# Kernel tuning notes

Measured on AMD Instinct MI355X. Metric: run time of the kernel, lower is better.

## Reference

```python
import jax, jax.numpy as jnp
import numpy as np

N_QUBITS = 8
C64 = jnp.complex64

# ---- gate matrices ----

def u3(t, p, l):
    c = jnp.cos(t / 2).astype(C64)
    s = jnp.sin(t / 2).astype(C64)
    ep = jnp.exp(1j * p).astype(C64)
    el = jnp.exp(1j * l).astype(C64)
    return jnp.stack([jnp.stack([c, -el * s]),
                      jnp.stack([ep * s, ep * el * c])])

def ry(t):
    c = jnp.cos(t / 2).astype(C64)
    s = jnp.sin(t / 2).astype(C64)
    return jnp.stack([jnp.stack([c, -s]), jnp.stack([s, c])])

def rz(t):
    e = jnp.exp(-0.5j * t).astype(C64)
    z = jnp.zeros((), C64)
    return jnp.stack([jnp.stack([e, z]), jnp.stack([z, jnp.conj(e)])])

CNOT = jnp.array([[1, 0, 0, 0], [0, 1, 0, 0], [0, 0, 0, 1], [0, 0, 1, 0]], C64)
PX = jnp.array([[0, 1], [1, 0]], C64)
PY = jnp.array([[0, -1j], [1j, 0]], C64)
PZ = jnp.array([[1, 0], [0, -1]], C64)

# ---- batched state-vector gate application; psi: [B] + [2]*8, wire 0 = axis 1 (MSB) ----

def apply_1q(psi, U, w):
    psi = jnp.moveaxis(psi, w + 1, -1)
    psi = psi @ U.T
    return jnp.moveaxis(psi, -1, w + 1)

def apply_2q(psi, U4, w0, w1):
    psi = jnp.moveaxis(psi, (w0 + 1, w1 + 1), (-2, -1))
    sh = psi.shape
    psi = (psi.reshape(sh[:-2] + (4,)) @ U4.T).reshape(sh)
    return jnp.moveaxis(psi, (-2, -1), (w0 + 1, w1 + 1))

def u_su4(psi, p, w0, w1):
    psi = apply_1q(psi, u3(p[0], p[1], p[2]), w0)
    psi = apply_1q(psi, u3(p[3], p[4], p[5]), w1)
    psi = apply_2q(psi, CNOT, w0, w1)
    psi = apply_1q(psi, ry(p[6]), w0)
    psi = apply_1q(psi, rz(p[7]), w1)
    psi = apply_2q(psi, CNOT, w1, w0)
    psi = apply_1q(psi, ry(p[8]), w0)
    psi = apply_2q(psi, CNOT, w0, w1)
    psi = apply_1q(psi, u3(p[9], p[10], p[11]), w0)
    psi = apply_1q(psi, u3(p[12], p[13], p[14]), w1)
    return psi

LAYER1 = [(0, 1), (2, 3), (4, 5), (6, 7), (1, 2), (3, 4), (5, 6), (7, 0)]
LAYER2 = [(2, 4), (6, 0), (0, 2), (4, 6)]
LAYER3 = [(2, 6)]

def expval(psi, ops):
    phi = psi
    for M, w in ops:
        phi = apply_1q(phi, M, w)
    return jnp.real(jnp.sum(jnp.conj(psi) * phi, axis=tuple(range(1, N_QUBITS + 1))))

def circuit(x, weights):
    # amplitude embedding with normalization
    psi = (x / jnp.linalg.norm(x, axis=1, keepdims=True)).astype(C64)
    psi = psi.reshape((x.shape[0],) + (2,) * N_QUBITS)
    npc = 15
    layers = [LAYER1, LAYER1, LAYER2, LAYER2, LAYER3]
    for i, wires in enumerate(layers):
        p = weights[i * npc:(i + 1) * npc]
        for (w0, w1) in wires:
            psi = u_su4(psi, p, w0, w1)
    meas = [
        expval(psi, [(PX, 2)]), expval(psi, [(PY, 2)]), expval(psi, [(PZ, 2)]),
        expval(psi, [(PX, 6)]), expval(psi, [(PY, 6)]), expval(psi, [(PZ, 6)]),
        expval(psi, [(PX, 2), (PX, 6)]),
        expval(psi, [(PY, 2), (PY, 6)]),
        expval(psi, [(PZ, 2), (PZ, 6)]),
    ]
    return jnp.stack(meas, axis=1)  # [B, 9]


def setup_inputs() -> dict:
    key = jax.random.key(0)
    k1, k2 = jax.random.split(key)
    x = jax.random.normal(k1, (8192, 256), dtype=jnp.float32)
    weights = jax.random.normal(k2, (75,), dtype=jnp.float32)
    return {"x": x, "weights": weights}


def reference(x, weights):
    return circuit(x, weights)
```

## Files before the change

kernel.cpp:

```cpp
#include <hip/hip_runtime.h>

typedef float2 c32;

__device__ __forceinline__ c32 cmul(c32 a, c32 b) {
    return make_float2(a.x * b.x - a.y * b.y, a.x * b.y + a.y * b.x);
}
__device__ __forceinline__ c32 cmad(c32 a, c32 b, c32 acc) {
    acc.x = fmaf(a.x, b.x, fmaf(-a.y, b.y, acc.x));
    acc.y = fmaf(a.x, b.y, fmaf(a.y, b.x, acc.y));
    return acc;
}


__device__ __forceinline__ void mk_u3(float th, float ph, float la, c32 U[2][2]) {
    float ct = cosf(0.5f * th), st = sinf(0.5f * th);
    U[0][0] = make_float2(ct, 0.f);
    U[0][1] = make_float2(-cosf(la) * st, -sinf(la) * st);
    U[1][0] = make_float2(cosf(ph) * st, sinf(ph) * st);
    U[1][1] = make_float2(cosf(ph + la) * ct, sinf(ph + la) * ct);
}

__device__ __forceinline__ void lmul_kron(const c32 A[2][2], const c32 B[2][2], c32 m[4]) {
    c32 t[4];
#pragma unroll
    for (int r = 0; r < 4; ++r) {
        c32 acc = make_float2(0.f, 0.f);
#pragma unroll
        for (int k = 0; k < 4; ++k)
            acc = cmad(cmul(A[r >> 1][k >> 1], B[r & 1][k & 1]), m[k], acc);
        t[r] = acc;
    }
#pragma unroll
    for (int r = 0; r < 4; ++r) m[r] = t[r];
}

__global__ void build_gates_kernel(const float* __restrict__ w, c32* __restrict__ mats) {
    const int t = threadIdx.x;
    if (t >= 20) return;
    const int g = t >> 2, c = t & 3;
    const float* p = w + g * 15;
    const int c0 = c >> 1, c1 = c & 1;
    c32 A[2][2], B[2][2], m[4], tmp;

    mk_u3(p[0], p[1], p[2], A);
    mk_u3(p[3], p[4], p[5], B);
#pragma unroll
    for (int r = 0; r < 4; ++r) m[r] = cmul(A[r >> 1][c0], B[r & 1][c1]);
    tmp = m[2]; m[2] = m[3]; m[3] = tmp;
    {
        float cc = cosf(0.5f * p[6]), s = sinf(0.5f * p[6]);
        A[0][0] = make_float2(cc, 0.f); A[0][1] = make_float2(-s, 0.f);
        A[1][0] = make_float2(s, 0.f);  A[1][1] = make_float2(cc, 0.f);
        float cz = cosf(0.5f * p[7]), sz = sinf(0.5f * p[7]);
        B[0][0] = make_float2(cz, -sz); B[0][1] = make_float2(0.f, 0.f);
        B[1][0] = make_float2(0.f, 0.f); B[1][1] = make_float2(cz, sz);
        lmul_kron(A, B, m);
    }
    tmp = m[1]; m[1] = m[3]; m[3] = tmp;
    {
        float cc = cosf(0.5f * p[8]), s = sinf(0.5f * p[8]);
        A[0][0] = make_float2(cc, 0.f); A[0][1] = make_float2(-s, 0.f);
        A[1][0] = make_float2(s, 0.f);  A[1][1] = make_float2(cc, 0.f);
        B[0][0] = make_float2(1.f, 0.f); B[0][1] = make_float2(0.f, 0.f);
        B[1][0] = make_float2(0.f, 0.f); B[1][1] = make_float2(1.f, 0.f);
        lmul_kron(A, B, m);
    }
    tmp = m[2]; m[2] = m[3]; m[3] = tmp;
    mk_u3(p[9], p[10], p[11], A);
    mk_u3(p[12], p[13], p[14], B);
    lmul_kron(A, B, m);
#pragma unroll
    for (int r = 0; r < 4; ++r) mats[g * 16 + r * 4 + c] = m[r];
}


#define STRIDE 516

__device__ __forceinline__ int swz8(int i) { return i ^ (i >> 4); }
__host__ __device__ constexpr int cswz8(int i) { return i ^ (i >> 4); }

template<int P3, int P2, int P1, int P0>
struct BitMap {
    __device__ static int scatterDyn(int v) {
        return (((v >> 3) & 1) << P3) | (((v >> 2) & 1) << P2) |
               (((v >> 1) & 1) << P1) | ((v & 1) << P0);
    }
    static constexpr int scatter(int v) {
        return (((v >> 3) & 1) << P3) | (((v >> 2) & 1) << P2) |
               (((v >> 1) & 1) << P1) | ((v & 1) << P0);
    }
};

using WA = BitMap<7, 6, 5, 4>;  using LA = BitMap<3, 2, 1, 0>;
using WB = BitMap<3, 2, 1, 0>;  using LB = BitMap<7, 6, 5, 4>;
using WC = BitMap<7, 4, 3, 0>;  using LC = BitMap<6, 5, 2, 1>;
using WD = BitMap<7, 5, 3, 1>;  using LD = BitMap<6, 4, 2, 0>;

template<class WO, class LO, class WN, class LN>
__device__ __forceinline__ void transition(c32* sl, int c, c32 s[16]) {
    const int uo = swz8(LO::scatterDyn(c));
#pragma unroll
    for (int r = 0; r < 16; ++r) sl[uo ^ cswz8(WO::scatter(r))] = s[r];
    const int un = swz8(LN::scatterDyn(c));
#pragma unroll
    for (int r = 0; r < 16; ++r) s[r] = sl[un ^ cswz8(WN::scatter(r))];
}

constexpr int freePos(int A, int B, int k) {
    int cnt = 0;
    for (int p = 0; p < 4; ++p)
        if (p != A && p != B) { if (cnt == k) return p; ++cnt; }
    return -1;
}

template<int A, int B>
__device__ __forceinline__ void gate(const c32 m[16], c32 s[16]) {
    constexpr int C0 = freePos(A, B, 0);
    constexpr int C1 = freePos(A, B, 1);
#pragma unroll
    for (int q = 0; q < 4; ++q) {
        const int base = ((q & 1) << C0) | (((q >> 1) & 1) << C1);
        const int i00 = base, i01 = base | (1 << B), i10 = base | (1 << A),
                  i11 = base | (1 << A) | (1 << B);
        c32 a0 = s[i00], a1 = s[i01], a2 = s[i10], a3 = s[i11];
        c32 r0 = cmul(m[0],  a0); r0 = cmad(m[1],  a1, r0); r0 = cmad(m[2],  a2, r0); r0 = cmad(m[3],  a3, r0);
        c32 r1 = cmul(m[4],  a0); r1 = cmad(m[5],  a1, r1); r1 = cmad(m[6],  a2, r1); r1 = cmad(m[7],  a3, r1);
        c32 r2 = cmul(m[8],  a0); r2 = cmad(m[9],  a1, r2); r2 = cmad(m[10], a2, r2); r2 = cmad(m[11], a3, r2);
        c32 r3 = cmul(m[12], a0); r3 = cmad(m[13], a1, r3); r3 = cmad(m[14], a2, r3); r3 = cmad(m[15], a3, r3);
        s[i00] = r0; s[i01] = r1; s[i10] = r2; s[i11] = r3;
    }
}

__device__ __forceinline__ void loadm(const c32* __restrict__ g, int idx, c32 m[16]) {
#pragma unroll
    for (int k = 0; k < 16; ++k) m[k] = g[idx * 16 + k];
}

__global__ __launch_bounds__(64) void sim_kernel(const float* __restrict__ x,
                                                 const c32* __restrict__ gmats,
                                                 float* __restrict__ out) {
    __shared__ c32 TR[4 * STRIDE];
    const int lane = threadIdx.x;
    const int st   = lane >> 4;
    const int c    = lane & 15;
    const int b    = blockIdx.x * 4 + st;

    const float* xb = x + (size_t)b * 256 + c;
    c32 s[16];
    float ss = 0.f;
#pragma unroll
    for (int r = 0; r < 16; ++r) {
        float v = xb[r << 4];
        s[r] = make_float2(v, 0.f);
        ss = fmaf(v, v, ss);
    }
#pragma unroll
    for (int o = 8; o; o >>= 1) ss += __shfl_xor(ss, o, 64);
    const float inv = 1.0f / sqrtf(ss);
#pragma unroll
    for (int r = 0; r < 16; ++r) s[r].x *= inv;

    c32* sl = TR + st * STRIDE;
    c32 m[16];

    loadm(gmats, 0, m);
    gate<3, 2>(m, s); gate<1, 0>(m, s); gate<2, 1>(m, s);
    transition<WA, LA, WB, LB>(sl, c, s);
    gate<3, 2>(m, s); gate<1, 0>(m, s); gate<2, 1>(m, s);
    transition<WB, LB, WC, LC>(sl, c, s);
    gate<2, 1>(m, s); gate<0, 3>(m, s);
    transition<WC, LC, WA, LA>(sl, c, s);
    loadm(gmats, 1, m);
    gate<3, 2>(m, s); gate<1, 0>(m, s); gate<2, 1>(m, s);
    transition<WA, LA, WB, LB>(sl, c, s);
    gate<3, 2>(m, s); gate<1, 0>(m, s); gate<2, 1>(m, s);
    transition<WB, LB, WC, LC>(sl, c, s);
    gate<2, 1>(m, s); gate<0, 3>(m, s);
    transition<WC, LC, WD, LD>(sl, c, s);
    loadm(gmats, 2, m);
    gate<2, 1>(m, s); gate<0, 3>(m, s); gate<3, 2>(m, s); gate<1, 0>(m, s);
    loadm(gmats, 3, m);
    gate<2, 1>(m, s); gate<0, 3>(m, s); gate<3, 2>(m, s); gate<1, 0>(m, s);
    loadm(gmats, 4, m);
    gate<2, 0>(m, s);

    float e0 = 0, e1 = 0, e2 = 0, e3 = 0, e4 = 0, e5 = 0, e6 = 0, e7 = 0, e8 = 0;
#pragma unroll
    for (int q = 0; q < 4; ++q) {
        const int f = ((q & 1) << 1) | ((q & 2) << 2);
        c32 a00 = s[f], a01 = s[f | 1], a10 = s[f | 4], a11 = s[f | 5];
        float n00 = a00.x * a00.x + a00.y * a00.y;
        float n01 = a01.x * a01.x + a01.y * a01.y;
        float n10 = a10.x * a10.x + a10.y * a10.y;
        float n11 = a11.x * a11.x + a11.y * a11.y;
        float z2r = a00.x * a10.x + a00.y * a10.y + a01.x * a11.x + a01.y * a11.y;
        float z2i = a00.x * a10.y - a00.y * a10.x + a01.x * a11.y - a01.y * a11.x;
        float z6r = a00.x * a01.x + a00.y * a01.y + a10.x * a11.x + a10.y * a11.y;
        float z6i = a00.x * a01.y - a00.y * a01.x + a10.x * a11.y - a10.y * a11.x;
        float w1r = a00.x * a11.x + a00.y * a11.y;
        float w2r = a01.x * a10.x + a01.y * a10.y;
        e0 += 2.f * z2r;  e1 += 2.f * z2i;  e2 += n00 + n01 - n10 - n11;
        e3 += 2.f * z6r;  e4 += 2.f * z6i;  e5 += n00 - n01 + n10 - n11;
        e6 += 2.f * (w1r + w2r);  e7 += 2.f * (w2r - w1r);
        e8 += n00 - n01 - n10 + n11;
    }
    float e[9] = {e0, e1, e2, e3, e4, e5, e6, e7, e8};
#pragma unroll
    for (int mm = 0; mm < 9; ++mm) {
        float v = e[mm];
#pragma unroll
        for (int o = 8; o; o >>= 1) v += __shfl_xor(v, o, 64);
        e[mm] = v;
    }
    if (c == 0) {
#pragma unroll
        for (int mm = 0; mm < 9; ++mm) out[b * 9 + mm] = e[mm];
    }
}

extern "C" void kernel_launch(void* const* d_in, const int* in_sizes, int n_in,
                              void* d_out, int out_size, void* d_ws, size_t ws_size,
                              hipStream_t stream) {
    const float* x = (const float*)d_in[0];
    const float* w = (const float*)d_in[1];
    float* out = (float*)d_out;
    c32* mats = (c32*)d_ws;

    hipLaunchKernelGGL(build_gates_kernel, dim3(1), dim3(64), 0, stream, w, mats);

    const int batch = in_sizes[0] / 256;
    const int nblocks = batch / 4;
    hipLaunchKernelGGL(sim_kernel, dim3(nblocks), dim3(64), 0, stream, x, mats, out);
}
```

Baseline: 32.74 us.

## Split each state vector over 32 lanes with 8 register amplitudes and XOR-swizzled transposes

Each batch element's 256 amplitudes are now spread over 32 lanes holding 8 amplitudes each, instead of 16 lanes holding 16. The gate schedule is rebuilt around 3-qubit register windows, with more LDS transpose steps that use per-transition XOR swizzles to avoid bank conflicts. Blocks grow to 256 threads covering 8 samples, with launch bounds set for 4 blocks per CU. The aim is lower register pressure and more threads in flight, at the cost of more shared-memory round trips per sample.

```diff
diff --git a/kernel.cpp b/kernel.cpp
--- a/kernel.cpp
+++ b/kernel.cpp
@@ -74,52 +74,72 @@
 }
 
 
-#define STRIDE 516
-
-__device__ __forceinline__ int swz8(int i) { return i ^ (i >> 4); }
-__host__ __device__ constexpr int cswz8(int i) { return i ^ (i >> 4); }
-
-template<int P3, int P2, int P1, int P0>
-struct BitMap {
-    __device__ static int scatterDyn(int v) {
-        return (((v >> 3) & 1) << P3) | (((v >> 2) & 1) << P2) |
-               (((v >> 1) & 1) << P1) | ((v & 1) << P0);
-    }
-    static constexpr int scatter(int v) {
-        return (((v >> 3) & 1) << P3) | (((v >> 2) & 1) << P2) |
-               (((v >> 1) & 1) << P1) | ((v & 1) << P0);
+template<int P2, int P1, int P0>
+struct Win {
+    static constexpr bool isReg(int p) { return p == P2 || p == P1 || p == P0; }
+    static constexpr int lanePos(int j) {
+        int cnt = 4;
+        for (int p = 7; p >= 0; --p)
+            if (!isReg(p)) { if (cnt == j) return p; --cnt; }
+        return -1;
+    }
+    __device__ __forceinline__ static int lane(int u) {
+        return (((u >> 4) & 1) << lanePos(4)) | (((u >> 3) & 1) << lanePos(3)) |
+               (((u >> 2) & 1) << lanePos(2)) | (((u >> 1) & 1) << lanePos(1)) |
+               ((u & 1) << lanePos(0));
+    }
+    static constexpr int reg(int r) {
+        return (((r >> 2) & 1) << P2) | (((r >> 1) & 1) << P1) | ((r & 1) << P0);
     }
 };
 
-using WA = BitMap<7, 6, 5, 4>;  using LA = BitMap<3, 2, 1, 0>;
-using WB = BitMap<3, 2, 1, 0>;  using LB = BitMap<7, 6, 5, 4>;
-using WC = BitMap<7, 4, 3, 0>;  using LC = BitMap<6, 5, 2, 1>;
-using WD = BitMap<7, 5, 3, 1>;  using LD = BitMap<6, 4, 2, 0>;
-
-template<class WO, class LO, class WN, class LN>
-__device__ __forceinline__ void transition(c32* sl, int c, c32 s[16]) {
-    const int uo = swz8(LO::scatterDyn(c));
-#pragma unroll
-    for (int r = 0; r < 16; ++r) sl[uo ^ cswz8(WO::scatter(r))] = s[r];
-    const int un = swz8(LN::scatterDyn(c));
-#pragma unroll
-    for (int r = 0; r < 16; ++r) s[r] = sl[un ^ cswz8(WN::scatter(r))];
-}
-
-constexpr int freePos(int A, int B, int k) {
-    int cnt = 0;
-    for (int p = 0; p < 4; ++p)
-        if (p != A && p != B) { if (cnt == k) return p; ++cnt; }
-    return -1;
+using WA_ = Win<7, 6, 5>;
+using WB_ = Win<6, 3, 2>;
+using WC_ = Win<7, 1, 0>;
+using WD_ = Win<5, 4, 3>;
+using WE_ = Win<7, 2, 1>;
+using WF_ = Win<6, 5, 3>;
+using WG_ = Win<7, 3, 1>;
+using WH_ = Win<7, 5, 3>;
+using WI_ = Win<7, 5, 1>;
+
+template<int S0, int T0, int S1, int T1, int S2, int T2, int S3, int T3>
+struct XF {
+    __device__ static constexpr int enc(int a) {
+        int x = a ^ (((a >> S0) & 1) << T0);
+        if constexpr (S1 >= 0) x ^= ((a >> S1) & 1) << T1;
+        if constexpr (S2 >= 0) x ^= ((a >> S2) & 1) << T2;
+        if constexpr (S3 >= 0) x ^= ((a >> S3) & 1) << T3;
+        return x;
+    }
+};
+using X1  = XF<7,3, 4,2, -1,-1, -1,-1>;
+using X2  = XF<7,3, 5,2, 6,1, 4,0>;
+using X3  = XF<7,3, 6,1, 5,0, -1,-1>;
+using X4  = XF<7,3, 5,2, 6,1, -1,-1>;
+using X5  = XF<4,2, 5,1, -1,-1, -1,-1>;
+using X10 = XF<7,3, 4,2, 5,1, -1,-1>;
+using X11 = XF<4,3, 6,1, -1,-1, -1,-1>;
+using X12 = XF<6,3, 4,1, -1,-1, -1,-1>;
+using X13 = XF<6,3, 5,1, -1,-1, -1,-1>;
+using X14 = XF<6,3, 4,1, -1,-1, -1,-1>;
+
+template<class WO, class WN, class X>
+__device__ __forceinline__ void trans(c32* sl, int u, c32 s[8]) {
+    const int lo = X::enc(WO::lane(u));
+#pragma unroll
+    for (int r = 0; r < 8; ++r) sl[lo ^ X::enc(WO::reg(r))] = s[r];
+    const int ln = X::enc(WN::lane(u));
+#pragma unroll
+    for (int r = 0; r < 8; ++r) s[r] = sl[ln ^ X::enc(WN::reg(r))];
 }
 
 template<int A, int B>
-__device__ __forceinline__ void gate(const c32 m[16], c32 s[16]) {
-    constexpr int C0 = freePos(A, B, 0);
-    constexpr int C1 = freePos(A, B, 1);
-#pragma unroll
-    for (int q = 0; q < 4; ++q) {
-        const int base = ((q & 1) << C0) | (((q >> 1) & 1) << C1);
+__device__ __forceinline__ void gate8(const c32 m[16], c32 s[8]) {
+    constexpr int Cb = 3 - A - B;
+#pragma unroll
+    for (int q = 0; q < 2; ++q) {
+        const int base = q << Cb;
         const int i00 = base, i01 = base | (1 << B), i10 = base | (1 << A),
                   i11 = base | (1 << A) | (1 << B);
         c32 a0 = s[i00], a1 = s[i01], a2 = s[i10], a3 = s[i11];
@@ -136,59 +156,83 @@
     for (int k = 0; k < 16; ++k) m[k] = g[idx * 16 + k];
 }
 
-__global__ __launch_bounds__(64) void sim_kernel(const float* __restrict__ x,
-                                                 const c32* __restrict__ gmats,
-                                                 float* __restrict__ out) {
-    __shared__ c32 TR[4 * STRIDE];
-    const int lane = threadIdx.x;
-    const int st   = lane >> 4;
-    const int c    = lane & 15;
-    const int b    = blockIdx.x * 4 + st;
-
-    const float* xb = x + (size_t)b * 256 + c;
-    c32 s[16];
+__global__ __launch_bounds__(256, 4) void sim_kernel(const float* __restrict__ x,
+                                                     const c32* __restrict__ gmats,
+                                                     float* __restrict__ out) {
+    __shared__ c32 TR[8 * 256];
+    const int tid = threadIdx.x;
+    const int wv = tid >> 6, lane = tid & 63;
+    const int st = lane >> 5, u = lane & 31;
+    const int slot = (wv << 1) | st;
+    const int b = blockIdx.x * 8 + slot;
+    c32* sl = TR + slot * 256;
+
+    const float* xr = x + (size_t)b * 256;
+    c32 s[8];
     float ss = 0.f;
 #pragma unroll
-    for (int r = 0; r < 16; ++r) {
-        float v = xb[r << 4];
+    for (int r = 0; r < 8; ++r) {
+        float v = xr[(r << 5) | u];
         s[r] = make_float2(v, 0.f);
         ss = fmaf(v, v, ss);
     }
 #pragma unroll
-    for (int o = 8; o; o >>= 1) ss += __shfl_xor(ss, o, 64);
+    for (int o = 16; o; o >>= 1) ss += __shfl_xor(ss, o, 64);
     const float inv = 1.0f / sqrtf(ss);
 #pragma unroll
-    for (int r = 0; r < 16; ++r) s[r].x *= inv;
-
-    c32* sl = TR + st * STRIDE;
+    for (int r = 0; r < 8; ++r) s[r].x *= inv;
+
     c32 m[16];
-
     loadm(gmats, 0, m);
-    gate<3, 2>(m, s); gate<1, 0>(m, s); gate<2, 1>(m, s);
-    transition<WA, LA, WB, LB>(sl, c, s);
-    gate<3, 2>(m, s); gate<1, 0>(m, s); gate<2, 1>(m, s);
-    transition<WB, LB, WC, LC>(sl, c, s);
-    gate<2, 1>(m, s); gate<0, 3>(m, s);
-    transition<WC, LC, WA, LA>(sl, c, s);
+    gate8<2, 1>(m, s);
+    trans<WA_, WB_, X1>(sl, u, s);
+    gate8<1, 0>(m, s);
+    trans<WB_, WC_, X2>(sl, u, s);
+    gate8<1, 0>(m, s);
+    gate8<0, 2>(m, s);
+    trans<WC_, WD_, X3>(sl, u, s);
+    gate8<2, 1>(m, s);
+    gate8<1, 0>(m, s);
+    trans<WD_, WE_, X4>(sl, u, s);
+    gate8<1, 0>(m, s);
+    trans<WE_, WA_, X5>(sl, u, s);
+    gate8<1, 0>(m, s);
     loadm(gmats, 1, m);
-    gate<3, 2>(m, s); gate<1, 0>(m, s); gate<2, 1>(m, s);
-    transition<WA, LA, WB, LB>(sl, c, s);
-    gate<3, 2>(m, s); gate<1, 0>(m, s); gate<2, 1>(m, s);
-    transition<WB, LB, WC, LC>(sl, c, s);
-    gate<2, 1>(m, s); gate<0, 3>(m, s);
-    transition<WC, LC, WD, LD>(sl, c, s);
+    gate8<2, 1>(m, s);
+    trans<WA_, WB_, X1>(sl, u, s);
+    gate8<1, 0>(m, s);
+    trans<WB_, WC_, X2>(sl, u, s);
+    gate8<1, 0>(m, s);
+    gate8<0, 2>(m, s);
+    trans<WC_, WD_, X3>(sl, u, s);
+    gate8<2, 1>(m, s);
+    gate8<1, 0>(m, s);
+    trans<WD_, WE_, X4>(sl, u, s);
+    gate8<1, 0>(m, s);
+    trans<WE_, WF_, X10>(sl, u, s);
+    gate8<2, 1>(m, s);
     loadm(gmats, 2, m);
-    gate<2, 1>(m, s); gate<0, 3>(m, s); gate<3, 2>(m, s); gate<1, 0>(m, s);
+    gate8<1, 0>(m, s);
+    trans<WF_, WG_, X11>(sl, u, s);
+    gate8<0, 2>(m, s);
+    gate8<1, 0>(m, s);
+    trans<WG_, WH_, X12>(sl, u, s);
+    gate8<2, 1>(m, s);
     loadm(gmats, 3, m);
-    gate<2, 1>(m, s); gate<0, 3>(m, s); gate<3, 2>(m, s); gate<1, 0>(m, s);
+    gate8<1, 0>(m, s);
+    trans<WH_, WG_, X13>(sl, u, s);
+    gate8<0, 2>(m, s);
+    gate8<1, 0>(m, s);
+    trans<WG_, WI_, X14>(sl, u, s);
+    gate8<2, 1>(m, s);
     loadm(gmats, 4, m);
-    gate<2, 0>(m, s);
+    gate8<1, 0>(m, s);
 
     float e0 = 0, e1 = 0, e2 = 0, e3 = 0, e4 = 0, e5 = 0, e6 = 0, e7 = 0, e8 = 0;
 #pragma unroll
-    for (int q = 0; q < 4; ++q) {
-        const int f = ((q & 1) << 1) | ((q & 2) << 2);
-        c32 a00 = s[f], a01 = s[f | 1], a10 = s[f | 4], a11 = s[f | 5];
+    for (int q = 0; q < 2; ++q) {
+        const int f = q << 2;
+        c32 a00 = s[f], a01 = s[f | 1], a10 = s[f | 2], a11 = s[f | 3];
         float n00 = a00.x * a00.x + a00.y * a00.y;
         float n01 = a01.x * a01.x + a01.y * a01.y;
         float n10 = a10.x * a10.x + a10.y * a10.y;
@@ -209,10 +253,10 @@
     for (int mm = 0; mm < 9; ++mm) {
         float v = e[mm];
 #pragma unroll
-        for (int o = 8; o; o >>= 1) v += __shfl_xor(v, o, 64);
+        for (int o = 16; o; o >>= 1) v += __shfl_xor(v, o, 64);
         e[mm] = v;
     }
-    if (c == 0) {
+    if (u == 0) {
 #pragma unroll
         for (int mm = 0; mm < 9; ++mm) out[b * 9 + mm] = e[mm];
     }
@@ -229,6 +273,6 @@
     hipLaunchKernelGGL(build_gates_kernel, dim3(1), dim3(64), 0, stream, w, mats);
 
     const int batch = in_sizes[0] / 256;
-    const int nblocks = batch / 4;
-    hipLaunchKernelGGL(sim_kernel, dim3(nblocks), dim3(64), 0, stream, x, mats, out);
-}
+    const int nblocks = batch / 8;
+    hipLaunchKernelGGL(sim_kernel, dim3(nblocks), dim3(256), 0, stream, x, mats, out);
+}
```

New measurement: 34.11 us. 1.04x slower.
